# Optimization experiments

Measured on AMD Instinct MI355X. Metric: run time of the kernel, lower is better.

The kernel has to match this reference:

```python
import jax, jax.numpy as jnp
import numpy as np
from jax.ops import segment_sum, segment_max

N, E, F, H, G, P, C = 50000, 600000, 128, 128, 64, 32, 10
HEADS = 3
BN_EPS = 1e-5
COS_EPS = 1e-8


def setup_inputs() -> dict:
    key = jax.random.key(0)
    ks = jax.random.split(key, 32)
    rn = lambda k, shape, s: jax.random.normal(k, shape, jnp.float32) * s
    inp = {
        "x": jax.random.normal(ks[0], (N, F), jnp.float32),
        "edge_index": jax.random.randint(ks[1], (2, E), 0, N, jnp.int32),
        "batch": jnp.sort(jax.random.randint(ks[2], (N,), 0, G, jnp.int32)),
        # GCNConv
        "W1": rn(ks[3], (F, H), F ** -0.5), "b1": jnp.zeros((H,), jnp.float32),
        # SAGEConv (lin_l on aggregated neighbors, lin_r on root)
        "Wl": rn(ks[4], (H, H), H ** -0.5), "Wr": rn(ks[5], (H, H), H ** -0.5),
        "bs": jnp.zeros((H,), jnp.float32),
        # GATConv, heads=3, concat=False
        "Wg": rn(ks[6], (H, HEADS * H), H ** -0.5),
        "a_src": rn(ks[7], (HEADS, H), H ** -0.5),
        "a_dst": rn(ks[8], (HEADS, H), H ** -0.5),
        "bg": jnp.zeros((H,), jnp.float32),
        # prototype head / classifier / decoder
        "protos": jax.random.normal(ks[9], (P, H), jnp.float32),
        "Wc": rn(ks[10], (H, C), H ** -0.5), "bc": jnp.zeros((C,), jnp.float32),
        "Wd1": rn(ks[11], (H, 2 * H), H ** -0.5), "bd1": jnp.zeros((2 * H,), jnp.float32),
        "Wd2": rn(ks[12], (2 * H, F), (2 * H) ** -0.5), "bd2": jnp.zeros((F,), jnp.float32),
    }
    # BatchNorm (eval mode): gamma, beta, running mean/var for bn1..bn3
    for i in range(3):
        k0, k1, k2 = jax.random.split(ks[13 + i], 3)
        inp[f"g{i+1}"] = 1.0 + rn(k0, (H,), 0.05)
        inp[f"be{i+1}"] = rn(k1, (H,), 0.05)
        inp[f"m{i+1}"] = rn(k2, (H,), 0.1)
        inp[f"v{i+1}"] = jnp.ones((H,), jnp.float32)
    return inp


def _bn(x, g, b, m, v):
    return (x - m) * jax.lax.rsqrt(v + BN_EPS) * g + b


def _forward(x, edge_index, batch,
             W1, b1, g1, be1, m1, v1,
             Wl, Wr, bs, g2, be2, m2, v2,
             Wg, a_src, a_dst, bg, g3, be3, m3, v3,
             protos, Wc, bc, Wd1, bd1, Wd2, bd2):
    src, dst = edge_index[0], edge_index[1]
    ones_e = jnp.ones((src.shape[0],), x.dtype)

    # --- GCNConv: symmetric norm with self-loops ---
    h = x @ W1                                        # [N, H]
    deg = segment_sum(ones_e, dst, num_segments=N) + 1.0
    dinv = jax.lax.rsqrt(deg)
    coef = dinv[src] * dinv[dst]                      # [E]
    h1 = segment_sum(h[src] * coef[:, None], dst, num_segments=N)
    h1 = h1 + h * (dinv * dinv)[:, None] + b1         # self-loop term + bias
    h1 = jax.nn.elu(_bn(h1, g1, be1, m1, v1))         # dropout = identity (eval)

    # --- SAGEConv: mean aggregation (no self-loops) ---
    cnt = segment_sum(ones_e, dst, num_segments=N)
    mean_nb = segment_sum(h1[src], dst, num_segments=N) / jnp.maximum(cnt, 1.0)[:, None]
    h2 = mean_nb @ Wl + h1 @ Wr + bs
    h2 = jax.nn.elu(_bn(h2, g2, be2, m2, v2))

    # --- GATConv: heads=3, concat=False (mean), with self-loops ---
    hg = (h2 @ Wg).reshape(N, HEADS, H)               # [N, 3, H]
    al_src = jnp.einsum('nhf,hf->nh', hg, a_src)      # [N, 3]
    al_dst = jnp.einsum('nhf,hf->nh', hg, a_dst)
    loop = jnp.arange(N, dtype=src.dtype)
    s2 = jnp.concatenate([src, loop])
    d2 = jnp.concatenate([dst, loop])
    e = jax.nn.leaky_relu(al_src[s2] + al_dst[d2], 0.2)   # [E+N, 3]
    emax = segment_max(e, d2, num_segments=N)             # every node has a self-loop
    ex = jnp.exp(e - emax[d2])
    den = segment_sum(ex, d2, num_segments=N)
    alpha = ex / den[d2]                                  # [E+N, 3]
    h3 = segment_sum(hg[s2] * alpha[:, :, None], d2, num_segments=N)
    h3 = h3.mean(axis=1) + bg                             # concat=False -> head mean
    h3 = jax.nn.elu(_bn(h3, g3, be3, m3, v3))

    # --- global mean pool over graphs ---
    gcnt = segment_sum(jnp.ones((N,), x.dtype), batch, num_segments=G)
    pooled = segment_sum(h3, batch, num_segments=G) / jnp.maximum(gcnt, 1.0)[:, None]

    # --- prototype head: cosine sim -> softmax -> mix ---
    xn = pooled / jnp.maximum(jnp.linalg.norm(pooled, axis=-1, keepdims=True), COS_EPS)
    pn = protos / jnp.maximum(jnp.linalg.norm(protos, axis=-1, keepdims=True), COS_EPS)
    sims = xn @ pn.T                                      # [G, P]
    assignments = jax.nn.softmax(sims, axis=-1)
    proto_emb = assignments @ protos                      # [G, H]
    logits = proto_emb @ Wc + bc                          # [G, C]
    reconstructed = jax.nn.relu(pooled @ Wd1 + bd1) @ Wd2 + bd2   # [G, F]
    return logits, proto_emb, assignments, reconstructed


def reference(x, edge_index, batch,
              W1, b1, g1, be1, m1, v1,
              Wl, Wr, bs, g2, be2, m2, v2,
              Wg, a_src, a_dst, bg, g3, be3, m3, v3,
              protos, Wc, bc, Wd1, bd1, Wd2, bd2):
    return _forward(x, edge_index, batch,
                    W1, b1, g1, be1, m1, v1,
                    Wl, Wr, bs, g2, be2, m2, v2,
                    Wg, a_src, a_dst, bg, g3, be3, m3, v3,
                    protos, Wc, bc, Wd1, bd1, Wd2, bd2)
```

## Files before the change

### kernel.cpp

```cpp
#include <hip/hip_runtime.h>
#include <hip/hip_bf16.h>
#include <stdint.h>
#include <stddef.h>

#define N_ 50000
#define E_ 600000
#define F_ 128
#define H_ 128
#define G_ 64
#define P_ 32
#define C_ 10
#define NB_ 49

typedef __hip_bfloat16 bf16;
typedef __attribute__((ext_vector_type(8))) short short8;
typedef __attribute__((ext_vector_type(4))) float float4v;

__device__ __forceinline__ float us2f(unsigned short u){ return __uint_as_float(((unsigned int)u)<<16); }
__device__ __forceinline__ unsigned short f2us(float x){ bf16 h = __float2bfloat16(x); return *(unsigned short*)&h; }
__device__ __forceinline__ float blo(unsigned int u){ return __uint_as_float(u<<16); }
__device__ __forceinline__ float bhi(unsigned int u){ return __uint_as_float(u & 0xFFFF0000u); }
__device__ __forceinline__ unsigned int packbf(float lo, float hi){ return ((unsigned int)f2us(hi)<<16) | f2us(lo); }
__device__ __forceinline__ float eluf(float x){ return x>0.f ? x : expm1f(x); }
__device__ __forceinline__ float bnf(float x,float m,float v,float g,float b){ return (x-m)*rsqrtf(v+1e-5f)*g+b; }
__device__ __forceinline__ float lrelu(float x){ return x>0.f ? x : 0.2f*x; }
__device__ __forceinline__ float expc(float x){ return __expf(fminf(x, 50.f)); }
__device__ __forceinline__ void atomAddF(float* a, float v){ unsafeAtomicAdd(a, v); }

__global__ __launch_bounds__(256) void k_wprep(const float* __restrict__ W1, const float* __restrict__ Wl,
    const float* __restrict__ Wr, const float* __restrict__ Wg, unsigned short* __restrict__ WT){
  int idx = blockIdx.x*256 + threadIdx.x;
  if(idx >= 6*16384) return;
  int m = idx >> 14, rem = idx & 16383;
  int n = rem >> 7, k = rem & 127;
  float v;
  if(m==0)      v = W1[k*128+n];
  else if(m==1) v = Wl[k*128+n];
  else if(m==2) v = Wr[k*128+n];
  else          v = Wg[k*384 + (m-3)*128 + n];
  WT[idx] = f2us(v);
}

__global__ __launch_bounds__(384) void k_vprep(const float* __restrict__ Wg, const float* __restrict__ a_src,
    const float* __restrict__ a_dst, float* __restrict__ vs3, float* __restrict__ vd3){
  int t = threadIdx.x;
  if(t >= 384) return;
  int h = t >> 7, f = t & 127;
  const float4* wr = (const float4*)(Wg + (size_t)f*384 + h*128);
  const float4* as = (const float4*)(a_src + h*128);
  const float4* ad = (const float4*)(a_dst + h*128);
  float s = 0.f, d = 0.f;
  #pragma unroll 8
  for(int j=0;j<32;j++){
    float4 wv = wr[j], av = as[j], dv = ad[j];
    s += wv.x*av.x + wv.y*av.y + wv.z*av.z + wv.w*av.w;
    d += wv.x*dv.x + wv.y*dv.y + wv.z*dv.z + wv.w*dv.w;
  }
  vs3[t] = s; vd3[t] = d;
}

__device__ __forceinline__ void stage_WT(const unsigned short* __restrict__ WTg, unsigned short* lds, int tid){
  #pragma unroll
  for(int i=0;i<8;i++){
    int idx = tid + i*256;
    int n = idx>>4, c = idx&15;
    uint4 v = *(const uint4*)(WTg + (size_t)idx*8);
    int cs = c ^ (n & 15);
    *(uint4*)(lds + n*128 + cs*8) = v;
  }
}
__device__ __forceinline__ short8 read_Bfrag(const unsigned short* lds, int tile, int kc, int lane){
  int n = tile*16 + (lane&15);
  int c = kc*4 + (lane>>4);
  int cs = c ^ (lane & 15);
  return *(const short8*)(lds + n*128 + cs*8);
}
__device__ __forceinline__ void load_Afrag_bf16(const bf16* A, int row, int lane, short8 af[4]){
  const unsigned short* ap = (const unsigned short*)A + (size_t)row*128 + (lane>>4)*8;
  #pragma unroll
  for(int kc=0;kc<4;kc++) af[kc] = *(const short8*)(ap + kc*32);
}
__device__ __forceinline__ void mfma_pass(const unsigned short* lds, const short8 af[4], int lane, float4v acc[8]){
  #pragma unroll
  for(int tile=0;tile<8;tile++){
    #pragma unroll
    for(int kc=0;kc<4;kc++){
      short8 bfv = read_Bfrag(lds, tile, kc, lane);
      acc[tile] = __builtin_amdgcn_mfma_f32_16x16x32_bf16(af[kc], bfv, acc[tile], 0, 0, 0);
    }
  }
}

__global__ __launch_bounds__(256) void k_mm_x(const float* __restrict__ X, const unsigned short* __restrict__ WTg,
                                              bf16* __restrict__ HB){
  __shared__ unsigned short Wlds[128*128];
  const int tid = threadIdx.x, lane = tid&63, w = tid>>6;
  const int row0 = blockIdx.x*64;
  stage_WT(WTg, Wlds, tid);
  int arow = row0 + w*16 + (lane&15);
  int ar = arow < N_ ? arow : N_-1;
  const float* ap = X + (size_t)ar*128 + (lane>>4)*8;
  short8 af[4];
  #pragma unroll
  for(int kc=0;kc<4;kc++){
    float4 a = *(const float4*)(ap + kc*32);
    float4 b = *(const float4*)(ap + kc*32 + 4);
    short8 v;
    v[0]=(short)f2us(a.x); v[1]=(short)f2us(a.y); v[2]=(short)f2us(a.z); v[3]=(short)f2us(a.w);
    v[4]=(short)f2us(b.x); v[5]=(short)f2us(b.y); v[6]=(short)f2us(b.z); v[7]=(short)f2us(b.w);
    af[kc]=v;
  }
  __syncthreads();
  float4v acc[8];
  #pragma unroll
  for(int t=0;t<8;t++){ acc[t][0]=0.f; acc[t][1]=0.f; acc[t][2]=0.f; acc[t][3]=0.f; }
  mfma_pass(Wlds, af, lane, acc);
  const int colb = lane&15, q = lane>>4;
  unsigned short* ob = (unsigned short*)HB;
  #pragma unroll
  for(int r=0;r<4;r++){
    int ro = row0 + w*16 + q*4 + r;
    if(ro < N_){
      #pragma unroll
      for(int tile=0;tile<8;tile++)
        ob[(size_t)ro*128 + tile*16 + colb] = f2us(acc[tile][r]);
    }
  }
}

__global__ __launch_bounds__(256) void k_sage_mm_att(const bf16* __restrict__ MaB, const bf16* __restrict__ H1B,
    const unsigned short* __restrict__ WlT, const unsigned short* __restrict__ WrT,
    const float* __restrict__ bs, const float* __restrict__ g2, const float* __restrict__ be2,
    const float* __restrict__ m2, const float* __restrict__ v2,
    const float* __restrict__ vs3, const float* __restrict__ vd3,
    bf16* __restrict__ H2B, float* __restrict__ als3, float* __restrict__ ald3){
  __shared__ unsigned short Wlds[128*128];
  const int tid = threadIdx.x, lane = tid&63, w = tid>>6;
  const int row0 = blockIdx.x*64;
  int arow = row0 + w*16 + (lane&15);
  int ar = arow < N_ ? arow : N_-1;
  float4v acc[8];
  #pragma unroll
  for(int t=0;t<8;t++){ acc[t][0]=0.f; acc[t][1]=0.f; acc[t][2]=0.f; acc[t][3]=0.f; }
  short8 af[4];

  stage_WT(WlT, Wlds, tid);
  load_Afrag_bf16(MaB, ar, lane, af);
  __syncthreads();
  mfma_pass(Wlds, af, lane, acc);
  __syncthreads();
  stage_WT(WrT, Wlds, tid);
  load_Afrag_bf16(H1B, ar, lane, af);
  __syncthreads();
  mfma_pass(Wlds, af, lane, acc);

  const int colb = lane&15, q = lane>>4;
  float vsv[24], vdv[24];
  #pragma unroll
  for(int h=0;h<3;h++){
    #pragma unroll
    for(int tile=0;tile<8;tile++){
      vsv[h*8+tile] = vs3[h*128 + tile*16 + colb];
      vdv[h*8+tile] = vd3[h*128 + tile*16 + colb];
    }
  }
  unsigned short* ob = (unsigned short*)H2B;
  #pragma unroll
  for(int tile=0;tile<8;tile++){
    int col = tile*16 + colb;
    float bsv=bs[col], gv=g2[col], bev=be2[col], mv=m2[col], vv=v2[col];
    #pragma unroll
    for(int r=0;r<4;r++){
      int ro = row0 + w*16 + q*4 + r;
      float x = eluf(bnf(acc[tile][r] + bsv, mv, vv, gv, bev));
      acc[tile][r] = x;
      if(ro < N_) ob[(size_t)ro*128 + col] = f2us(x);
    }
  }
  #pragma unroll
  for(int r=0;r<4;r++){
    int ro = row0 + w*16 + q*4 + r;
    #pragma unroll
    for(int h=0;h<3;h++){
      float ps=0.f, pd=0.f;
      #pragma unroll
      for(int tile=0;tile<8;tile++){ ps += acc[tile][r]*vsv[h*8+tile]; pd += acc[tile][r]*vdv[h*8+tile]; }
      #pragma unroll
      for(int o=8;o>0;o>>=1){ ps += __shfl_down(ps,o,16); pd += __shfl_down(pd,o,16); }
      if(colb==0 && ro<N_){ als3[ro*3+h] = ps; ald3[ro*3+h] = pd; }
    }
  }
}

__global__ __launch_bounds__(256) void k_gat_mm3(const bf16* __restrict__ U, const unsigned short* __restrict__ WgT,
    const float* __restrict__ bg, const float* __restrict__ g3, const float* __restrict__ be3,
    const float* __restrict__ m3, const float* __restrict__ v3, bf16* __restrict__ H3B){
  __shared__ unsigned short Wlds[128*128];
  const int tid = threadIdx.x, lane = tid&63, w = tid>>6;
  const int row0 = blockIdx.x*64;
  int arow = row0 + w*16 + (lane&15);
  int ar = arow < N_ ? arow : N_-1;
  float4v acc[8];
  #pragma unroll
  for(int t=0;t<8;t++){ acc[t][0]=0.f; acc[t][1]=0.f; acc[t][2]=0.f; acc[t][3]=0.f; }
  short8 af[4];
  for(int hh=0; hh<3; hh++){
    if(hh) __syncthreads();
    stage_WT(WgT + hh*16384, Wlds, tid);
    const unsigned short* ap = (const unsigned short*)U + (size_t)ar*384 + hh*128 + (lane>>4)*8;
    #pragma unroll
    for(int kc=0;kc<4;kc++) af[kc] = *(const short8*)(ap + kc*32);
    __syncthreads();
    mfma_pass(Wlds, af, lane, acc);
  }
  const int colb = lane&15, q = lane>>4;
  unsigned short* ob = (unsigned short*)H3B;
  #pragma unroll
  for(int tile=0;tile<8;tile++){
    int col = tile*16 + colb;
    float bgv=bg[col], gv=g3[col], bev=be3[col], mv=m3[col], vv=v3[col];
    #pragma unroll
    for(int r=0;r<4;r++){
      int ro = row0 + w*16 + q*4 + r;
      if(ro < N_){
        float x = acc[tile][r] + bgv;
        ob[(size_t)ro*128 + col] = f2us(eluf(bnf(x, mv, vv, gv, bev)));
      }
    }
  }
}

__global__ __launch_bounds__(256) void k_count(const int* __restrict__ dst, int* __restrict__ cnt){
  int e = blockIdx.x*256 + threadIdx.x;
  if(e < E_) atomicAdd(&cnt[dst[e]], 1);
}

__global__ __launch_bounds__(1024) void k_scan1(const int* __restrict__ cnt, int* __restrict__ row_ptr,
                                                float* __restrict__ dinv, int* __restrict__ bsum){
  __shared__ int wsum[16];
  const int t = threadIdx.x, lane = t & 63, wid = t >> 6;
  int i = blockIdx.x*1024 + t;
  int v = (i<N_) ? cnt[i] : 0;
  int x = v;
  #pragma unroll
  for(int o=1;o<64;o<<=1){
    int y = __shfl_up(x, o, 64);
    if(lane >= o) x += y;
  }
  if(lane==63) wsum[wid] = x;
  __syncthreads();
  if(wid==0){
    int s = (lane<16) ? wsum[lane] : 0;
    #pragma unroll
    for(int o=1;o<16;o<<=1){
      int y = __shfl_up(s, o, 64);
      if(lane >= o) s += y;
    }
    if(lane<16) wsum[lane] = s;
  }
  __syncthreads();
  int waveoff = (wid>0) ? wsum[wid-1] : 0;
  int incl = waveoff + x;
  if(i<N_){
    row_ptr[i] = incl - v;
    dinv[i] = rsqrtf((float)v + 1.f);
  }
  if(t==1023) bsum[blockIdx.x] = incl;
}

__global__ __launch_bounds__(64) void k_scan2(const int* __restrict__ bsum, int* __restrict__ boff,
                                              int* __restrict__ row_ptr){
  int lane = threadIdx.x;
  int v = (lane < NB_) ? bsum[lane] : 0;
  int x = v;
  #pragma unroll
  for(int o=1;o<64;o<<=1){
    int y = __shfl_up(x, o, 64);
    if(lane >= o) x += y;
  }
  if(lane < NB_) boff[lane] = x - v;
  if(lane == 63) row_ptr[N_] = x;
}

__global__ __launch_bounds__(256) void k_scan3(int* __restrict__ row_ptr, const int* __restrict__ boff,
                                               int* __restrict__ tmp){
  int i = blockIdx.x*256 + threadIdx.x;
  if(i < N_){
    int r = row_ptr[i] + boff[i>>10];
    row_ptr[i] = r;
    tmp[i] = r;
  }
}

__global__ __launch_bounds__(256) void k_scatter(const int* __restrict__ src, const int* __restrict__ dst,
                                                 int* __restrict__ tmp, int* __restrict__ esrc,
                                                 int* __restrict__ edst){
  int e = blockIdx.x*256 + threadIdx.x;
  if(e < E_){
    int d = dst[e];
    int pos = atomicAdd(&tmp[d], 1);
    esrc[pos] = src[e];
    edst[pos] = d;
  }
}

__global__ __launch_bounds__(256) void k_wexp(const int* __restrict__ esrc, const int* __restrict__ edst,
    const float* __restrict__ als3, const float* __restrict__ ald3, float* __restrict__ we4){
  int e = blockIdx.x*256 + threadIdx.x;
  if(e >= E_) return;
  int s = esrc[e], d = edst[e];
  float4 w;
  w.x = expc(lrelu(als3[s*3+0] + ald3[d*3+0]));
  w.y = expc(lrelu(als3[s*3+1] + ald3[d*3+1]));
  w.z = expc(lrelu(als3[s*3+2] + ald3[d*3+2]));
  w.w = 0.f;
  *(float4*)(we4 + (size_t)e*4) = w;
}

__global__ __launch_bounds__(256) void k_gcn_gather(const int* __restrict__ row_ptr, const int* __restrict__ esrc,
    const float* __restrict__ dinv, const bf16* __restrict__ HB,
    const float* __restrict__ b1, const float* __restrict__ g1, const float* __restrict__ be1,
    const float* __restrict__ m1, const float* __restrict__ v1, bf16* __restrict__ H1B){
  int n = blockIdx.x*4 + (threadIdx.x>>6);
  int lane = threadIdx.x & 63;
  if(n >= N_) return;
  int beg = row_ptr[n], end = row_ptr[n+1];
  float dn = dinv[n];
  float a0 = 0.f, a1 = 0.f;
  const unsigned short* hb = (const unsigned short*)HB;
  int e = beg;
  for(; e+3 < end; e += 4){
    int s0 = esrc[e], s1 = esrc[e+1], s2 = esrc[e+2], s3 = esrc[e+3];
    unsigned int hv0 = *(const unsigned int*)(hb + (size_t)s0*H_ + lane*2);
    unsigned int hv1 = *(const unsigned int*)(hb + (size_t)s1*H_ + lane*2);
    unsigned int hv2 = *(const unsigned int*)(hb + (size_t)s2*H_ + lane*2);
    unsigned int hv3 = *(const unsigned int*)(hb + (size_t)s3*H_ + lane*2);
    float c0 = dinv[s0]*dn, c1 = dinv[s1]*dn, c2 = dinv[s2]*dn, c3 = dinv[s3]*dn;
    a0 += c0*blo(hv0) + c1*blo(hv1) + c2*blo(hv2) + c3*blo(hv3);
    a1 += c0*bhi(hv0) + c1*bhi(hv1) + c2*bhi(hv2) + c3*bhi(hv3);
  }
  for(; e < end; e++){
    int s = esrc[e];
    float c = dinv[s]*dn;
    unsigned int hv = *(const unsigned int*)(hb + (size_t)s*H_ + lane*2);
    a0 += c*blo(hv);
    a1 += c*bhi(hv);
  }
  unsigned int hv = *(const unsigned int*)(hb + (size_t)n*H_ + lane*2);
  int f0 = lane*2, f1 = f0+1;
  float x0 = a0 + blo(hv)*dn*dn + b1[f0];
  float x1 = a1 + bhi(hv)*dn*dn + b1[f1];
  x0 = eluf(bnf(x0, m1[f0], v1[f0], g1[f0], be1[f0]));
  x1 = eluf(bnf(x1, m1[f1], v1[f1], g1[f1], be1[f1]));
  unsigned int o = ((unsigned int)f2us(x1)<<16) | f2us(x0);
  *(unsigned int*)((unsigned short*)H1B + (size_t)n*H_ + lane*2) = o;
}

__global__ __launch_bounds__(256) void k_sage_gather(const int* __restrict__ row_ptr, const int* __restrict__ esrc,
    const bf16* __restrict__ H1B, bf16* __restrict__ MeanB){
  int n = blockIdx.x*4 + (threadIdx.x>>6);
  int lane = threadIdx.x & 63;
  if(n >= N_) return;
  int beg = row_ptr[n], end = row_ptr[n+1];
  float a0 = 0.f, a1 = 0.f;
  const unsigned short* hb = (const unsigned short*)H1B;
  int e = beg;
  for(; e+3 < end; e += 4){
    int s0 = esrc[e], s1 = esrc[e+1], s2 = esrc[e+2], s3 = esrc[e+3];
    unsigned int hv0 = *(const unsigned int*)(hb + (size_t)s0*H_ + lane*2);
    unsigned int hv1 = *(const unsigned int*)(hb + (size_t)s1*H_ + lane*2);
    unsigned int hv2 = *(const unsigned int*)(hb + (size_t)s2*H_ + lane*2);
    unsigned int hv3 = *(const unsigned int*)(hb + (size_t)s3*H_ + lane*2);
    a0 += blo(hv0) + blo(hv1) + blo(hv2) + blo(hv3);
    a1 += bhi(hv0) + bhi(hv1) + bhi(hv2) + bhi(hv3);
  }
  for(; e < end; e++){
    unsigned int hv = *(const unsigned int*)(hb + (size_t)esrc[e]*H_ + lane*2);
    a0 += blo(hv);
    a1 += bhi(hv);
  }
  float inv = 1.f / fmaxf((float)(end-beg), 1.f);
  unsigned int o = ((unsigned int)f2us(a1*inv)<<16) | f2us(a0*inv);
  *(unsigned int*)((unsigned short*)MeanB + (size_t)n*H_ + lane*2) = o;
}

__global__ __launch_bounds__(256) void k_gat_agg(const int* __restrict__ row_ptr, const int* __restrict__ esrc,
    const float* __restrict__ als3, const float* __restrict__ ald3, const float* __restrict__ we4,
    const bf16* __restrict__ H2B, bf16* __restrict__ U){
  int n = blockIdx.x*4 + (threadIdx.x>>6);
  int lane = threadIdx.x & 63;
  if(n >= N_) return;
  int beg = row_ptr[n], end = row_ptr[n+1];
  float es0 = expc(lrelu(als3[n*3+0] + ald3[n*3+0]));
  float es1 = expc(lrelu(als3[n*3+1] + ald3[n*3+1]));
  float es2 = expc(lrelu(als3[n*3+2] + ald3[n*3+2]));
  const unsigned short* hb = (const unsigned short*)H2B;
  unsigned int xs = *(const unsigned int*)(hb + (size_t)n*H_ + lane*2);
  float x0 = blo(xs), x1 = bhi(xs);
  float den0 = es0, den1 = es1, den2 = es2;
  float a00 = es0*x0, a01 = es0*x1;
  float a10 = es1*x0, a11 = es1*x1;
  float a20 = es2*x0, a21 = es2*x1;
  int e = beg;
  for(; e+3 < end; e += 4){
    int s0 = esrc[e], s1 = esrc[e+1], s2 = esrc[e+2], s3 = esrc[e+3];
    float4 w0 = *(const float4*)(we4 + (size_t)(e  )*4);
    float4 w1 = *(const float4*)(we4 + (size_t)(e+1)*4);
    float4 w2 = *(const float4*)(we4 + (size_t)(e+2)*4);
    float4 w3 = *(const float4*)(we4 + (size_t)(e+3)*4);
    unsigned int p0 = *(const unsigned int*)(hb + (size_t)s0*H_ + lane*2);
    unsigned int p1 = *(const unsigned int*)(hb + (size_t)s1*H_ + lane*2);
    unsigned int p2 = *(const unsigned int*)(hb + (size_t)s2*H_ + lane*2);
    unsigned int p3 = *(const unsigned int*)(hb + (size_t)s3*H_ + lane*2);
    den0 += w0.x + w1.x + w2.x + w3.x;
    den1 += w0.y + w1.y + w2.y + w3.y;
    den2 += w0.z + w1.z + w2.z + w3.z;
    float q00=blo(p0), q01=bhi(p0), q10=blo(p1), q11=bhi(p1);
    float q20=blo(p2), q21=bhi(p2), q30=blo(p3), q31=bhi(p3);
    a00 += w0.x*q00 + w1.x*q10 + w2.x*q20 + w3.x*q30;
    a01 += w0.x*q01 + w1.x*q11 + w2.x*q21 + w3.x*q31;
    a10 += w0.y*q00 + w1.y*q10 + w2.y*q20 + w3.y*q30;
    a11 += w0.y*q01 + w1.y*q11 + w2.y*q21 + w3.y*q31;
    a20 += w0.z*q00 + w1.z*q10 + w2.z*q20 + w3.z*q30;
    a21 += w0.z*q01 + w1.z*q11 + w2.z*q21 + w3.z*q31;
  }
  for(; e < end; e++){
    int s = esrc[e];
    float4 w = *(const float4*)(we4 + (size_t)e*4);
    unsigned int p = *(const unsigned int*)(hb + (size_t)s*H_ + lane*2);
    float q0 = blo(p), q1 = bhi(p);
    den0 += w.x; den1 += w.y; den2 += w.z;
    a00 += w.x*q0; a01 += w.x*q1;
    a10 += w.y*q0; a11 += w.y*q1;
    a20 += w.z*q0; a21 += w.z*q1;
  }
  float i0 = 1.f/(3.f*den0), i1 = 1.f/(3.f*den1), i2 = 1.f/(3.f*den2);
  unsigned short* ub = (unsigned short*)U;
  size_t ubase = (size_t)n*384 + lane*2;
  *(unsigned int*)(ub + ubase)       = packbf(a00*i0, a01*i0);
  *(unsigned int*)(ub + ubase + 128) = packbf(a10*i1, a11*i1);
  *(unsigned int*)(ub + ubase + 256) = packbf(a20*i2, a21*i2);
}

#define NPW_ 16
__global__ __launch_bounds__(256) void k_h3pool(const bf16* __restrict__ H3B,
    const int* __restrict__ batch, float* __restrict__ pooled, float* __restrict__ gcnt){
  int wave = blockIdx.x*4 + (threadIdx.x>>6);
  int lane = threadIdx.x & 63;
  int n0 = wave*NPW_;
  if(n0 >= N_) return;
  int n1 = n0 + NPW_; if(n1 > N_) n1 = N_;
  int f0 = lane*2, f1 = f0+1;
  float r0=0.f, r1=0.f;
  int cur = batch[n0];
  int seg = 0;
  for(int n=n0; n<n1; n++){
    int b = batch[n];
    if(b != cur){
      atomAddF(&pooled[cur*H_ + f0], r0);
      atomAddF(&pooled[cur*H_ + f1], r1);
      if(lane==0) atomAddF(&gcnt[cur], (float)seg);
      r0 = 0.f; r1 = 0.f; seg = 0; cur = b;
    }
    unsigned int hv = *(const unsigned int*)((const unsigned short*)H3B + (size_t)n*H_ + lane*2);
    r0 += blo(hv);
    r1 += bhi(hv);
    seg++;
  }
  atomAddF(&pooled[cur*H_ + f0], r0);
  atomAddF(&pooled[cur*H_ + f1], r1);
  if(lane==0) atomAddF(&gcnt[cur], (float)seg);
}

__global__ __launch_bounds__(128) void k_head(const float* __restrict__ pooledacc, const float* __restrict__ gcnt,
    const float* __restrict__ protos, const float* __restrict__ Wc, const float* __restrict__ bc,
    const float* __restrict__ Wd1, const float* __restrict__ bd1, const float* __restrict__ Wd2, const float* __restrict__ bd2,
    float* __restrict__ out){
  const int g = blockIdx.x, t = threadIdx.x;
  __shared__ float p[128], xn[128], red[128], sims[32], es[32], asg[32], pe[128], t1[256];
  __shared__ float nrm;
  float cg_ = fmaxf(gcnt[g], 1.f);
  p[t] = pooledacc[g*128 + t] / cg_;
  __syncthreads();
  red[t] = p[t]*p[t];
  __syncthreads();
  for(int s=64;s>0;s>>=1){ if(t<s) red[t]+=red[t+s]; __syncthreads(); }
  if(t==0) nrm = fmaxf(sqrtf(red[0]), 1e-8f);
  __syncthreads();
  xn[t] = p[t]/nrm;
  __syncthreads();
  if(t<32){
    float s=0.f, pn=0.f;
    for(int f=0;f<128;f++){ float pv=protos[t*128+f]; s += xn[f]*pv; pn += pv*pv; }
    sims[t] = s / fmaxf(sqrtf(pn), 1e-8f);
  }
  __syncthreads();
  if(t<32){
    float mx=-1e30f;
    for(int j=0;j<32;j++) mx = fmaxf(mx, sims[j]);
    es[t] = __expf(sims[t]-mx);
  }
  __syncthreads();
  if(t<32){
    float sm=0.f;
    for(int j=0;j<32;j++) sm += es[j];
    float a = es[t]/fmaxf(sm,1e-20f);
    asg[t] = a;
    out[8832 + g*32 + t] = a;
  }
  __syncthreads();
  {
    float s=0.f;
    for(int pp=0;pp<32;pp++) s += asg[pp]*protos[pp*128+t];
    pe[t] = s;
    out[640 + g*128 + t] = s;
  }
  __syncthreads();
  if(t<10){
    float s = bc[t];
    for(int f=0;f<128;f++) s += pe[f]*Wc[f*10+t];
    out[g*10 + t] = s;
  }
  for(int j=t;j<256;j+=128){
    float s = bd1[j];
    for(int f=0;f<128;f++) s += p[f]*Wd1[f*256+j];
    t1[j] = fmaxf(s, 0.f);
  }
  __syncthreads();
  {
    float s = bd2[t];
    for(int j=0;j<256;j++) s += t1[j]*Wd2[j*128+t];
    out[10880 + g*128 + t] = s;
  }
}

__global__ void k_sentinel(float* out, float code){
  out[0] = code;
}

extern "C" void kernel_launch(void* const* d_in, const int* in_sizes, int n_in,
                              void* d_out, int out_size, void* d_ws, size_t ws_size,
                              hipStream_t stream){
  const float* X    = (const float*)d_in[0];
  const int*  EI    = (const int*)d_in[1];
  const int*  batch = (const int*)d_in[2];
  const int* src = EI;
  const int* dst = EI + E_;

  int iW1,ib1,iWl,iWr,ibs,iWg,ias,iad,ibg,ipr,iWc,ibc,iWd1,ibd1,iWd2,ibd2;
  int ig1,ibe1,im1,iv1,ig2,ibe2,im2,iv2,ig3,ibe3,im3,iv3;
  if(n_in >= 31 && in_sizes[5] == 128){
    iW1=3; ib1=4; ig1=5; ibe1=6; im1=7; iv1=8;
    iWl=9; iWr=10; ibs=11; ig2=12; ibe2=13; im2=14; iv2=15;
    iWg=16; ias=17; iad=18; ibg=19; ig3=20; ibe3=21; im3=22; iv3=23;
    ipr=24; iWc=25; ibc=26; iWd1=27; ibd1=28; iWd2=29; ibd2=30;
  }else{
    iW1=3; ib1=4; iWl=5; iWr=6; ibs=7; iWg=8; ias=9; iad=10; ibg=11;
    ipr=12; iWc=13; ibc=14; iWd1=15; ibd1=16; iWd2=17; ibd2=18;
    ig1=19; ibe1=20; im1=21; iv1=22; ig2=23; ibe2=24; im2=25; iv2=26;
    ig3=27; ibe3=28; im3=29; iv3=30;
  }
  const float* W1 = (const float*)d_in[iW1];   const float* b1 = (const float*)d_in[ib1];
  const float* Wl = (const float*)d_in[iWl];   const float* Wr = (const float*)d_in[iWr];
  const float* bs = (const float*)d_in[ibs];   const float* Wg = (const float*)d_in[iWg];
  const float* a_src = (const float*)d_in[ias]; const float* a_dst = (const float*)d_in[iad];
  const float* bg = (const float*)d_in[ibg];   const float* protos = (const float*)d_in[ipr];
  const float* Wc = (const float*)d_in[iWc];   const float* bc = (const float*)d_in[ibc];
  const float* Wd1 = (const float*)d_in[iWd1]; const float* bd1 = (const float*)d_in[ibd1];
  const float* Wd2 = (const float*)d_in[iWd2]; const float* bd2 = (const float*)d_in[ibd2];
  const float* g1 = (const float*)d_in[ig1];   const float* be1 = (const float*)d_in[ibe1];
  const float* m1 = (const float*)d_in[im1];   const float* v1 = (const float*)d_in[iv1];
  const float* g2 = (const float*)d_in[ig2];   const float* be2 = (const float*)d_in[ibe2];
  const float* m2 = (const float*)d_in[im2];   const float* v2 = (const float*)d_in[iv2];
  const float* g3 = (const float*)d_in[ig3];   const float* be3 = (const float*)d_in[ibe3];
  const float* m3 = (const float*)d_in[im3];   const float* v3 = (const float*)d_in[iv3];

  const size_t NF = (size_t)N_*H_;
  const size_t intN = (size_t)3*N_ + 4 + (size_t)2*E_ + 128;
  const size_t fltN = (size_t)7*N_ + (size_t)4*E_ + G_*H_ + G_ + 768;
  const size_t NEED = NF*2*3 + (size_t)N_*384*2 + intN*4 + fltN*4 + (size_t)6*16384*2;
  if(ws_size < NEED){
    k_sentinel<<<1,1,0,stream>>>((float*)d_out, 1000.f + (float)(ws_size>>20));
    return;
  }
  bf16* RA = (bf16*)d_ws;
  bf16* RB = RA + NF;
  bf16* RC = RB + NF;
  bf16* U  = RC + NF;
  int*  cnt     = (int*)(U + (size_t)N_*384);
  int*  row_ptr = cnt + N_;
  int*  tmp     = row_ptr + (N_+4);
  int*  esrc    = tmp + N_;
  int*  edst    = esrc + E_;
  int*  bsum    = edst + E_;
  int*  boff    = bsum + 64;
  float* dinv   = (float*)(boff + 64);
  float* als3   = dinv + N_;
  float* ald3   = als3 + (size_t)N_*3;
  float* we4    = ald3 + (size_t)N_*3;
  float* pooled = we4 + (size_t)E_*4;
  float* gcnt   = pooled + (size_t)G_*H_;
  float* vs3    = gcnt + G_;
  float* vd3    = vs3 + 384;
  unsigned short* WTg = (unsigned short*)(vd3 + 384);

  k_wprep<<<(6*16384+255)/256, 256, 0, stream>>>(W1, Wl, Wr, Wg, WTg);
  k_vprep<<<1, 384, 0, stream>>>(Wg, a_src, a_dst, vs3, vd3);
  hipMemsetAsync(cnt, 0, N_*sizeof(int), stream);
  k_count<<<(E_+255)/256, 256, 0, stream>>>(dst, cnt);
  k_scan1<<<NB_, 1024, 0, stream>>>(cnt, row_ptr, dinv, bsum);
  k_scan2<<<1, 64, 0, stream>>>(bsum, boff, row_ptr);
  k_scan3<<<(N_+255)/256, 256, 0, stream>>>(row_ptr, boff, tmp);
  k_scatter<<<(E_+255)/256, 256, 0, stream>>>(src, dst, tmp, esrc, edst);

  const int GB = (N_+3)/4;
  const int MB = (N_+63)/64;
  k_mm_x<<<MB, 256, 0, stream>>>(X, WTg, RA);
  k_gcn_gather<<<GB, 256, 0, stream>>>(row_ptr, esrc, dinv, RA, b1, g1, be1, m1, v1, RB);
  k_sage_gather<<<GB, 256, 0, stream>>>(row_ptr, esrc, RB, RC);
  k_sage_mm_att<<<MB, 256, 0, stream>>>(RC, RB, WTg + 16384, WTg + 2*16384, bs, g2, be2, m2, v2,
                                        vs3, vd3, RA, als3, ald3);
  k_wexp<<<(E_+255)/256, 256, 0, stream>>>(esrc, edst, als3, ald3, we4);
  k_gat_agg<<<GB, 256, 0, stream>>>(row_ptr, esrc, als3, ald3, we4, RA, U);
  k_gat_mm3<<<MB, 256, 0, stream>>>(U, WTg + 3*16384, bg, g3, be3, m3, v3, RC);
  hipMemsetAsync(pooled, 0, (size_t)(G_*H_+G_)*sizeof(float), stream);
  {
    int waves = (N_ + NPW_ - 1)/NPW_;
    int blocks = (waves + 3)/4;
    k_h3pool<<<blocks, 256, 0, stream>>>(RC, batch, pooled, gcnt);
  }
  k_head<<<G_, 128, 0, stream>>>(pooled, gcnt, protos, Wc, bc, Wd1, bd1, Wd2, bd2, (float*)d_out);
}
```

Baseline: 438.0 us.

## Pre-swizzle weights into MFMA fragment order and read B directly from global

The weight-prep kernel now writes weights in per-lane MFMA B-fragment order. The three dense matmul kernels drop their LDS staging and barriers and load B fragments straight from global memory, where they are L2-cached and coalesced. This removes 32KB of LDS per block and the sync overhead, which should raise occupancy, at the cost of repeated global/L2 reads of the weights by every block. ELU also switches from expm1f to __expf-1, which is cheaper but less accurate near zero.

New measurement: 427.5 us. 2.4% less time.

```diff
diff --git a/kernel.cpp b/kernel.cpp
--- a/kernel.cpp
+++ b/kernel.cpp
@@ -21,7 +21,7 @@
 __device__ __forceinline__ float blo(unsigned int u){ return __uint_as_float(u<<16); }
 __device__ __forceinline__ float bhi(unsigned int u){ return __uint_as_float(u & 0xFFFF0000u); }
 __device__ __forceinline__ unsigned int packbf(float lo, float hi){ return ((unsigned int)f2us(hi)<<16) | f2us(lo); }
-__device__ __forceinline__ float eluf(float x){ return x>0.f ? x : expm1f(x); }
+__device__ __forceinline__ float eluf(float x){ return x>0.f ? x : __expf(x)-1.f; }
 __device__ __forceinline__ float bnf(float x,float m,float v,float g,float b){ return (x-m)*rsqrtf(v+1e-5f)*g+b; }
 __device__ __forceinline__ float lrelu(float x){ return x>0.f ? x : 0.2f*x; }
 __device__ __forceinline__ float expc(float x){ return __expf(fminf(x, 50.f)); }
@@ -31,8 +31,13 @@
     const float* __restrict__ Wr, const float* __restrict__ Wg, unsigned short* __restrict__ WT){
   int idx = blockIdx.x*256 + threadIdx.x;
   if(idx >= 6*16384) return;
-  int m = idx >> 14, rem = idx & 16383;
-  int n = rem >> 7, k = rem & 127;
+  int m    = idx >> 14;
+  int tile = (idx >> 11) & 7;
+  int kc   = (idx >> 9) & 3;
+  int lane = (idx >> 3) & 63;
+  int j    = idx & 7;
+  int k = kc*32 + (lane>>4)*8 + j;
+  int n = tile*16 + (lane&15);
   float v;
   if(m==0)      v = W1[k*128+n];
   else if(m==1) v = Wl[k*128+n];
@@ -59,33 +64,18 @@
   vs3[t] = s; vd3[t] = d;
 }
 
-__device__ __forceinline__ void stage_WT(const unsigned short* __restrict__ WTg, unsigned short* lds, int tid){
-  #pragma unroll
-  for(int i=0;i<8;i++){
-    int idx = tid + i*256;
-    int n = idx>>4, c = idx&15;
-    uint4 v = *(const uint4*)(WTg + (size_t)idx*8);
-    int cs = c ^ (n & 15);
-    *(uint4*)(lds + n*128 + cs*8) = v;
-  }
-}
-__device__ __forceinline__ short8 read_Bfrag(const unsigned short* lds, int tile, int kc, int lane){
-  int n = tile*16 + (lane&15);
-  int c = kc*4 + (lane>>4);
-  int cs = c ^ (lane & 15);
-  return *(const short8*)(lds + n*128 + cs*8);
-}
 __device__ __forceinline__ void load_Afrag_bf16(const bf16* A, int row, int lane, short8 af[4]){
   const unsigned short* ap = (const unsigned short*)A + (size_t)row*128 + (lane>>4)*8;
   #pragma unroll
   for(int kc=0;kc<4;kc++) af[kc] = *(const short8*)(ap + kc*32);
 }
-__device__ __forceinline__ void mfma_pass(const unsigned short* lds, const short8 af[4], int lane, float4v acc[8]){
+__device__ __forceinline__ void mfma_pass_g(const unsigned short* __restrict__ WB, const short8 af[4],
+                                            int lane, float4v acc[8]){
   #pragma unroll
   for(int tile=0;tile<8;tile++){
     #pragma unroll
     for(int kc=0;kc<4;kc++){
-      short8 bfv = read_Bfrag(lds, tile, kc, lane);
+      short8 bfv = *(const short8*)(WB + (((tile*4+kc)*64 + lane)<<3));
       acc[tile] = __builtin_amdgcn_mfma_f32_16x16x32_bf16(af[kc], bfv, acc[tile], 0, 0, 0);
     }
   }
@@ -93,10 +83,8 @@
 
 __global__ __launch_bounds__(256) void k_mm_x(const float* __restrict__ X, const unsigned short* __restrict__ WTg,
                                               bf16* __restrict__ HB){
-  __shared__ unsigned short Wlds[128*128];
   const int tid = threadIdx.x, lane = tid&63, w = tid>>6;
   const int row0 = blockIdx.x*64;
-  stage_WT(WTg, Wlds, tid);
   int arow = row0 + w*16 + (lane&15);
   int ar = arow < N_ ? arow : N_-1;
   const float* ap = X + (size_t)ar*128 + (lane>>4)*8;
@@ -110,11 +98,10 @@
     v[4]=(short)f2us(b.x); v[5]=(short)f2us(b.y); v[6]=(short)f2us(b.z); v[7]=(short)f2us(b.w);
     af[kc]=v;
   }
-  __syncthreads();
   float4v acc[8];
   #pragma unroll
   for(int t=0;t<8;t++){ acc[t][0]=0.f; acc[t][1]=0.f; acc[t][2]=0.f; acc[t][3]=0.f; }
-  mfma_pass(Wlds, af, lane, acc);
+  mfma_pass_g(WTg, af, lane, acc);
   const int colb = lane&15, q = lane>>4;
   unsigned short* ob = (unsigned short*)HB;
   #pragma unroll
@@ -129,12 +116,11 @@
 }
 
 __global__ __launch_bounds__(256) void k_sage_mm_att(const bf16* __restrict__ MaB, const bf16* __restrict__ H1B,
-    const unsigned short* __restrict__ WlT, const unsigned short* __restrict__ WrT,
+    const unsigned short* __restrict__ WlF, const unsigned short* __restrict__ WrF,
     const float* __restrict__ bs, const float* __restrict__ g2, const float* __restrict__ be2,
     const float* __restrict__ m2, const float* __restrict__ v2,
     const float* __restrict__ vs3, const float* __restrict__ vd3,
     bf16* __restrict__ H2B, float* __restrict__ als3, float* __restrict__ ald3){
-  __shared__ unsigned short Wlds[128*128];
   const int tid = threadIdx.x, lane = tid&63, w = tid>>6;
   const int row0 = blockIdx.x*64;
   int arow = row0 + w*16 + (lane&15);
@@ -143,16 +129,10 @@
   #pragma unroll
   for(int t=0;t<8;t++){ acc[t][0]=0.f; acc[t][1]=0.f; acc[t][2]=0.f; acc[t][3]=0.f; }
   short8 af[4];
-
-  stage_WT(WlT, Wlds, tid);
   load_Afrag_bf16(MaB, ar, lane, af);
-  __syncthreads();
-  mfma_pass(Wlds, af, lane, acc);
-  __syncthreads();
-  stage_WT(WrT, Wlds, tid);
+  mfma_pass_g(WlF, af, lane, acc);
   load_Afrag_bf16(H1B, ar, lane, af);
-  __syncthreads();
-  mfma_pass(Wlds, af, lane, acc);
+  mfma_pass_g(WrF, af, lane, acc);
 
   const int colb = lane&15, q = lane>>4;
   float vsv[24], vdv[24];
@@ -192,10 +172,9 @@
   }
 }
 
-__global__ __launch_bounds__(256) void k_gat_mm3(const bf16* __restrict__ U, const unsigned short* __restrict__ WgT,
+__global__ __launch_bounds__(256) void k_gat_mm3(const bf16* __restrict__ U, const unsigned short* __restrict__ WgF,
     const float* __restrict__ bg, const float* __restrict__ g3, const float* __restrict__ be3,
     const float* __restrict__ m3, const float* __restrict__ v3, bf16* __restrict__ H3B){
-  __shared__ unsigned short Wlds[128*128];
   const int tid = threadIdx.x, lane = tid&63, w = tid>>6;
   const int row0 = blockIdx.x*64;
   int arow = row0 + w*16 + (lane&15);
@@ -205,13 +184,10 @@
   for(int t=0;t<8;t++){ acc[t][0]=0.f; acc[t][1]=0.f; acc[t][2]=0.f; acc[t][3]=0.f; }
   short8 af[4];
   for(int hh=0; hh<3; hh++){
-    if(hh) __syncthreads();
-    stage_WT(WgT + hh*16384, Wlds, tid);
     const unsigned short* ap = (const unsigned short*)U + (size_t)ar*384 + hh*128 + (lane>>4)*8;
     #pragma unroll
     for(int kc=0;kc<4;kc++) af[kc] = *(const short8*)(ap + kc*32);
-    __syncthreads();
-    mfma_pass(Wlds, af, lane, acc);
+    mfma_pass_g(WgF + hh*16384, af, lane, acc);
   }
   const int colb = lane&15, q = lane>>4;
   unsigned short* ob = (unsigned short*)H3B;
```
